# Kernel tuning notes

Hardware: AMD Instinct MI355X
Metric: run time of the kernel (lower is better)

The kernel has to match this reference:

```python
import jax, jax.numpy as jnp
import numpy as np

B, H, KVH, HD, S = 16, 32, 8, 128, 4096
D = H * HD  # 4096
Q = 1  # decode: one query token per batch element


def rotate_half(x):
    half = x.shape[-1] // 2
    return jnp.concatenate([-x[..., half:], x[..., :half]], axis=-1)


def setup_inputs() -> dict:
    key = jax.random.key(0)
    ks = jax.random.split(key, 8)
    hidden_states = jax.random.normal(ks[0], (B, Q, D), dtype=jnp.float32)
    current_steps = jax.random.randint(ks[1], (B,), 0, S - 1)
    # additive causal mask per batch: positions <= current_step visible
    pos = jnp.arange(S)[None, :]
    attention_mask = jnp.where(pos <= current_steps[:, None], 0.0, -1e9).astype(jnp.float32)[:, None, None, :]  # [B,1,1,S]
    # RoPE cos/sin at each batch element's current position
    inv_freq = 1.0 / (10000.0 ** (jnp.arange(0, HD, 2, dtype=jnp.float32) / HD))
    ang = current_steps[:, None].astype(jnp.float32) * inv_freq[None, :]  # [B, HD/2]
    ang = jnp.concatenate([ang, ang], axis=-1)  # [B, HD]
    cos = jnp.cos(ang)[:, None, None, :]  # [B,1,1,HD]
    sin = jnp.sin(ang)[:, None, None, :]
    past_key = jax.random.normal(ks[2], (B, KVH, S, HD), dtype=jnp.float32)
    past_value = jax.random.normal(ks[3], (B, KVH, S, HD), dtype=jnp.float32)
    sc = 1.0 / np.sqrt(D)
    Wq = jax.random.normal(ks[4], (D, H * HD), dtype=jnp.float32) * sc
    Wk = jax.random.normal(ks[5], (D, KVH * HD), dtype=jnp.float32) * sc
    Wv = jax.random.normal(ks[6], (D, KVH * HD), dtype=jnp.float32) * sc
    Wo = jax.random.normal(ks[7], (H * HD, D), dtype=jnp.float32) * sc
    return dict(hidden_states=hidden_states, attention_mask=attention_mask,
                current_steps=current_steps, cos=cos, sin=sin,
                past_key=past_key, past_value=past_value,
                Wq=Wq, Wk=Wk, Wv=Wv, Wo=Wo)


def reference(hidden_states, attention_mask, current_steps, cos, sin,
              past_key, past_value, Wq, Wk, Wv, Wo):
    b, q_len, d = hidden_states.shape
    # projections -> [B, heads, Q, HD]
    q = (hidden_states @ Wq).reshape(b, q_len, H, HD).transpose(0, 2, 1, 3)
    k = (hidden_states @ Wk).reshape(b, q_len, KVH, HD).transpose(0, 2, 1, 3)
    v = (hidden_states @ Wv).reshape(b, q_len, KVH, HD).transpose(0, 2, 1, 3)
    # RoPE
    q = q * cos + rotate_half(q) * sin
    k = k * cos + rotate_half(k) * sin
    # KV-cache scatter at current_step per batch (slice_scatter equivalent)
    def upd(cache_b, new_b, step):
        return jax.lax.dynamic_update_slice(cache_b, new_b, (0, step, 0))
    new_key = jax.vmap(upd)(past_key, k, current_steps)      # [B,KVH,S,HD]
    new_value = jax.vmap(upd)(past_value, v, current_steps)  # [B,KVH,S,HD]
    # GQA attention
    g = H // KVH
    qg = q.reshape(b, KVH, g, q_len, HD)
    scores = jnp.einsum('bkgqd,bksd->bkgqs', qg, new_key) / np.sqrt(HD)
    scores = scores + attention_mask[:, :, None, :, :]  # [B,1,1,Q,S] broadcast
    probs = jax.nn.softmax(scores, axis=-1)
    out = jnp.einsum('bkgqs,bksd->bkgqd', probs, new_value)
    out = out.reshape(b, H, q_len, HD).transpose(0, 2, 1, 3).reshape(b, q_len, H * HD)
    attn_out = out @ Wo
    return attn_out, new_key, new_value
```

## Files before the change

kernel.cpp:

```cpp
#include <hip/hip_runtime.h>

#define B 16
#define H 32
#define KVH 8
#define HD 128
#define S 4096
#define D 4096
#define NQKV 6144
#define PSPLIT 32
#define WSPLIT 32
#define NCH 16
#define CROWS (S / NCH)
#define SCALE 0.08838834764831845f

__global__ void k_proj(const float* __restrict__ hs, const float* __restrict__ Wq,
                       const float* __restrict__ Wk, const float* __restrict__ Wv,
                       float* __restrict__ part) {
  int n = blockIdx.x * 256 + threadIdx.x;
  int k0 = blockIdx.y * (D / PSPLIT);
  const float* w; int ldw, col;
  if (n < 4096)      { w = Wq; ldw = 4096; col = n; }
  else if (n < 5120) { w = Wk; ldw = 1024; col = n - 4096; }
  else               { w = Wv; ldw = 1024; col = n - 5120; }
  float acc[B];
#pragma unroll
  for (int b = 0; b < B; b++) acc[b] = 0.f;
  const float* wp = w + (size_t)k0 * ldw + col;
#pragma unroll 8
  for (int k = 0; k < D / PSPLIT; k++) {
    float wv = wp[(size_t)k * ldw];
#pragma unroll
    for (int b = 0; b < B; b++) acc[b] = fmaf(hs[b * D + k0 + k], wv, acc[b]);
  }
  float* p = part + (size_t)blockIdx.y * (B * NQKV);
#pragma unroll
  for (int b = 0; b < B; b++) p[(size_t)b * NQKV + n] = acc[b];
}

__global__ void k_reduce_rope(const float* __restrict__ part, const float* __restrict__ cosb,
                              const float* __restrict__ sinb, const int* __restrict__ steps,
                              float* __restrict__ qr, float* __restrict__ nkrow,
                              float* __restrict__ nvrow) {
  int i = blockIdx.x * 256 + threadIdx.x;
  int b = i / NQKV, n = i % NQKV;
  float v = 0.f;
#pragma unroll
  for (int c = 0; c < PSPLIT; c++) v += part[(size_t)c * B * NQKV + (size_t)b * NQKV + n];
  if (n < 5120) {
    int d = n & 127;
    int pn = (d < 64) ? n + 64 : n - 64;
    float pv = 0.f;
#pragma unroll
    for (int c = 0; c < PSPLIT; c++) pv += part[(size_t)c * B * NQKV + (size_t)b * NQKV + pn];
    float rot = (d < 64) ? -pv : pv;
    float r = v * cosb[b * HD + d] + rot * sinb[b * HD + d];
    if (n < 4096) qr[(size_t)b * D + n] = r;
    else          nkrow[(size_t)b * KVH * HD + (n - 4096)] = r;
  } else {
    nvrow[(size_t)b * KVH * HD + (n - 5120)] = v;
  }
}

__global__ void k_fusedK(const float* __restrict__ pastk, const float* __restrict__ nkrow,
                         const float* __restrict__ qr, const int* __restrict__ steps,
                         float* __restrict__ newk, float* __restrict__ scores) {
  int ch = blockIdx.x, kvh = blockIdx.y, b = blockIdx.z;
  int t = threadIdx.x;
  int ln = t & 15, rg = t >> 4;
  int s0 = ch * CROWS;
  int step = steps[b];
  int L = step + 1;
  int h0 = kvh * 4;
  const float4* qbase = (const float4*)(qr + ((size_t)b * H + h0) * HD);
  float4 q0[4], q1[4];
#pragma unroll
  for (int h = 0; h < 4; h++) {
    q0[h] = qbase[h * 32 + ln];
    q1[h] = qbase[h * 32 + ln + 16];
  }
  const float4* subp = (const float4*)(nkrow + (size_t)(b * KVH + kvh) * HD);
  float4 sub0 = subp[ln], sub1 = subp[ln + 16];
  const float4* src = (const float4*)(pastk + ((size_t)(b * KVH + kvh) * S + s0) * HD);
  float4*       dst = (float4*)(newk + ((size_t)(b * KVH + kvh) * S + s0) * HD);
  float* srow = scores + (size_t)(b * H + h0) * S + s0;
#pragma unroll 4
  for (int it = 0; it < CROWS / 16; ++it) {
    int row = it * 16 + rg;
    size_t o0 = (size_t)row * 32 + ln;
    float4 k0 = src[o0];
    float4 k1 = src[o0 + 16];
    if (s0 + row == step) { k0 = sub0; k1 = sub1; }
    dst[o0] = k0;
    dst[o0 + 16] = k1;
    if (s0 + row < L) {
      float a0, a1, a2, a3;
      a0 = fmaf(k0.x, q0[0].x, fmaf(k0.y, q0[0].y, fmaf(k0.z, q0[0].z, fmaf(k0.w, q0[0].w,
           fmaf(k1.x, q1[0].x, fmaf(k1.y, q1[0].y, fmaf(k1.z, q1[0].z, k1.w * q1[0].w)))))));
      a1 = fmaf(k0.x, q0[1].x, fmaf(k0.y, q0[1].y, fmaf(k0.z, q0[1].z, fmaf(k0.w, q0[1].w,
           fmaf(k1.x, q1[1].x, fmaf(k1.y, q1[1].y, fmaf(k1.z, q1[1].z, k1.w * q1[1].w)))))));
      a2 = fmaf(k0.x, q0[2].x, fmaf(k0.y, q0[2].y, fmaf(k0.z, q0[2].z, fmaf(k0.w, q0[2].w,
           fmaf(k1.x, q1[2].x, fmaf(k1.y, q1[2].y, fmaf(k1.z, q1[2].z, k1.w * q1[2].w)))))));
      a3 = fmaf(k0.x, q0[3].x, fmaf(k0.y, q0[3].y, fmaf(k0.z, q0[3].z, fmaf(k0.w, q0[3].w,
           fmaf(k1.x, q1[3].x, fmaf(k1.y, q1[3].y, fmaf(k1.z, q1[3].z, k1.w * q1[3].w)))))));
#pragma unroll
      for (int o = 1; o < 16; o <<= 1) {
        a0 += __shfl_xor(a0, o);
        a1 += __shfl_xor(a1, o);
        a2 += __shfl_xor(a2, o);
        a3 += __shfl_xor(a3, o);
      }
      if (ln < 4) {
        float my = (ln == 0) ? a0 : (ln == 1) ? a1 : (ln == 2) ? a2 : a3;
        srow[(size_t)ln * S + row] = my * SCALE;
      }
    }
  }
}

__global__ void k_smax(float* __restrict__ scores, const int* __restrict__ steps) {
  int bid = blockIdx.x;
  int b = bid >> 5, h = bid & 31;
  int t = threadIdx.x;
  __shared__ float red[4];
  int L = steps[b] + 1;
  float* srow = scores + (size_t)(b * H + h) * S;
  float lmax = -1e30f;
  for (int s = t; s < L; s += 256) lmax = fmaxf(lmax, srow[s]);
#pragma unroll
  for (int o = 32; o > 0; o >>= 1) lmax = fmaxf(lmax, __shfl_xor(lmax, o));
  if ((t & 63) == 0) red[t >> 6] = lmax;
  __syncthreads();
  float gm = fmaxf(fmaxf(red[0], red[1]), fmaxf(red[2], red[3]));
  float lsum = 0.f;
  for (int s = t; s < L; s += 256) {
    float p = __expf(srow[s] - gm);
    srow[s] = p;
    lsum += p;
  }
#pragma unroll
  for (int o = 32; o > 0; o >>= 1) lsum += __shfl_xor(lsum, o);
  __syncthreads();
  if ((t & 63) == 0) red[t >> 6] = lsum;
  __syncthreads();
  float inv = 1.f / (red[0] + red[1] + red[2] + red[3]);
  for (int s = t; s < L; s += 256) srow[s] *= inv;
}

__global__ void k_fusedV(const float* __restrict__ pastv, const float* __restrict__ nvrow,
                         const float* __restrict__ probs, const int* __restrict__ steps,
                         float* __restrict__ newv, float* __restrict__ part) {
  int ch = blockIdx.x, kvh = blockIdx.y, b = blockIdx.z;
  int t = threadIdx.x;
  int d4 = t & 31, rr = t >> 5;
  int s0 = ch * CROWS;
  int step = steps[b];
  int L = step + 1;
  int h0 = kvh * 4;
  float4 subv = ((const float4*)(nvrow + (size_t)(b * KVH + kvh) * HD))[d4];
  const float4* src = (const float4*)(pastv + ((size_t)(b * KVH + kvh) * S + s0) * HD);
  float4*       dst = (float4*)(newv + ((size_t)(b * KVH + kvh) * S + s0) * HD);
  const float* pb = probs + (size_t)(b * H + h0) * S + s0;
  float4 a0 = make_float4(0.f, 0.f, 0.f, 0.f), a1 = a0, a2 = a0, a3 = a0;
#pragma unroll 4
  for (int i = 0; i < CROWS / 8; ++i) {
    int r = i * 8 + rr;
    float4 v = src[r * 32 + d4];
    if (s0 + r == step) v = subv;
    dst[r * 32 + d4] = v;
    if (s0 + r < L) {
      float q0 = pb[r], q1 = pb[S + r], q2 = pb[2 * S + r], q3 = pb[3 * S + r];
      a0.x = fmaf(q0, v.x, a0.x); a0.y = fmaf(q0, v.y, a0.y);
      a0.z = fmaf(q0, v.z, a0.z); a0.w = fmaf(q0, v.w, a0.w);
      a1.x = fmaf(q1, v.x, a1.x); a1.y = fmaf(q1, v.y, a1.y);
      a1.z = fmaf(q1, v.z, a1.z); a1.w = fmaf(q1, v.w, a1.w);
      a2.x = fmaf(q2, v.x, a2.x); a2.y = fmaf(q2, v.y, a2.y);
      a2.z = fmaf(q2, v.z, a2.z); a2.w = fmaf(q2, v.w, a2.w);
      a3.x = fmaf(q3, v.x, a3.x); a3.y = fmaf(q3, v.y, a3.y);
      a3.z = fmaf(q3, v.z, a3.z); a3.w = fmaf(q3, v.w, a3.w);
    }
  }
  a0.x += __shfl_xor(a0.x, 32); a0.y += __shfl_xor(a0.y, 32);
  a0.z += __shfl_xor(a0.z, 32); a0.w += __shfl_xor(a0.w, 32);
  a1.x += __shfl_xor(a1.x, 32); a1.y += __shfl_xor(a1.y, 32);
  a1.z += __shfl_xor(a1.z, 32); a1.w += __shfl_xor(a1.w, 32);
  a2.x += __shfl_xor(a2.x, 32); a2.y += __shfl_xor(a2.y, 32);
  a2.z += __shfl_xor(a2.z, 32); a2.w += __shfl_xor(a2.w, 32);
  a3.x += __shfl_xor(a3.x, 32); a3.y += __shfl_xor(a3.y, 32);
  a3.z += __shfl_xor(a3.z, 32); a3.w += __shfl_xor(a3.w, 32);
  __shared__ float4 red[4][4][32];
  int w = t >> 6;
  if ((t & 32) == 0) {
    red[w][0][d4] = a0; red[w][1][d4] = a1; red[w][2][d4] = a2; red[w][3][d4] = a3;
  }
  __syncthreads();
  if (t < 128) {
    int hh = t >> 5, dd = t & 31;
    float4 x0 = red[0][hh][dd], x1 = red[1][hh][dd], x2 = red[2][hh][dd], x3 = red[3][hh][dd];
    float4 s;
    s.x = (x0.x + x1.x) + (x2.x + x3.x);
    s.y = (x0.y + x1.y) + (x2.y + x3.y);
    s.z = (x0.z + x1.z) + (x2.z + x3.z);
    s.w = (x0.w + x1.w) + (x2.w + x3.w);
    ((float4*)(part + (((size_t)ch * B + b) * KVH + kvh) * 512))[t] = s;
  }
}

__global__ void k_reduce_ctx(const float* __restrict__ part, float* __restrict__ ctx) {
  int i = blockIdx.x * 256 + threadIdx.x;
  int b = i >> 12, r = i & 4095, h = r >> 7, d = r & 127;
  int kvh = h >> 2, hl = h & 3;
  float s = 0.f;
#pragma unroll
  for (int c = 0; c < NCH; c++)
    s += part[(((size_t)c * B + b) * KVH + kvh) * 512 + hl * 128 + d];
  ctx[i] = s;
}

__global__ void k_wo(const float* __restrict__ ctx, const float* __restrict__ Wo,
                     float* __restrict__ part) {
  int n = blockIdx.x * 256 + threadIdx.x;
  int k0 = blockIdx.y * (D / WSPLIT);
  float acc[B];
#pragma unroll
  for (int b = 0; b < B; b++) acc[b] = 0.f;
  const float* wp = Wo + (size_t)k0 * D + n;
#pragma unroll 8
  for (int k = 0; k < D / WSPLIT; k++) {
    float wv = wp[(size_t)k * D];
#pragma unroll
    for (int b = 0; b < B; b++) acc[b] = fmaf(ctx[b * D + k0 + k], wv, acc[b]);
  }
  float* p = part + (size_t)blockIdx.y * (B * D);
#pragma unroll
  for (int b = 0; b < B; b++) p[(size_t)b * D + n] = acc[b];
}

__global__ void k_reduce_out(const float* __restrict__ part, float* __restrict__ out) {
  int i = blockIdx.x * 256 + threadIdx.x;
  float s = 0.f;
#pragma unroll
  for (int c = 0; c < WSPLIT; c++) s += part[(size_t)c * B * D + i];
  out[i] = s;
}

extern "C" void kernel_launch(void* const* d_in, const int* in_sizes, int n_in,
                              void* d_out, int out_size, void* d_ws, size_t ws_size,
                              hipStream_t stream) {
  const float* hs    = (const float*)d_in[0];
  const int*   steps = (const int*)d_in[2];
  const float* cosb  = (const float*)d_in[3];
  const float* sinb  = (const float*)d_in[4];
  const float* pk    = (const float*)d_in[5];
  const float* pvv   = (const float*)d_in[6];
  const float* Wq    = (const float*)d_in[7];
  const float* Wk    = (const float*)d_in[8];
  const float* Wv    = (const float*)d_in[9];
  const float* Wo    = (const float*)d_in[10];

  float* attn_out = (float*)d_out;
  float* newk = attn_out + (size_t)B * D;
  float* newv = newk + (size_t)B * KVH * S * HD;

  float* ws = (float*)d_ws;
  float* A        = ws;
  float* p_part   = A;
  float* p_scores = A;
  float* p_wopart = A;
  float* p_pvpart = A + 3145728;
  float* p_qr     = p_pvpart + 1048576;
  float* p_nkrow  = p_qr + (size_t)B * D;
  float* p_nvrow  = p_nkrow + (size_t)B * KVH * HD;
  float* p_ctx    = p_nvrow + (size_t)B * KVH * HD;

  hipLaunchKernelGGL(k_proj, dim3(NQKV / 256, PSPLIT), dim3(256), 0, stream,
                     hs, Wq, Wk, Wv, p_part);
  hipLaunchKernelGGL(k_reduce_rope, dim3(B * NQKV / 256), dim3(256), 0, stream,
                     p_part, cosb, sinb, steps, p_qr, p_nkrow, p_nvrow);
  hipLaunchKernelGGL(k_fusedK, dim3(NCH, KVH, B), dim3(256), 0, stream,
                     pk, p_nkrow, p_qr, steps, newk, p_scores);
  hipLaunchKernelGGL(k_smax, dim3(B * H), dim3(256), 0, stream,
                     p_scores, steps);
  hipLaunchKernelGGL(k_fusedV, dim3(NCH, KVH, B), dim3(256), 0, stream,
                     pvv, p_nvrow, p_scores, steps, newv, p_pvpart);
  hipLaunchKernelGGL(k_reduce_ctx, dim3(B * D / 256), dim3(256), 0, stream,
                     p_pvpart, p_ctx);
  hipLaunchKernelGGL(k_wo, dim3(D / 256, WSPLIT), dim3(256), 0, stream,
                     p_ctx, Wo, p_wopart);
  hipLaunchKernelGGL(k_reduce_out, dim3(B * D / 256), dim3(256), 0, stream,
                     p_wopart, attn_out);
}
```

Baseline: 343.4 us.

## Use nontemporal KV streaming and stage scores and probs through LDS

The K and V cache copy-and-attend kernels now read past KV and write new KV with nontemporal loads and stores, so the streaming traffic does less to pollute the caches. Scores are collected in a shared-memory tile and written out row-coalesced at the end of each chunk. Probabilities are preloaded into shared memory once per block instead of being fetched from global memory for every row. Per-row causal guards become wave-uniform per-iteration guards, which adds extra compute and some harmless garbage score writes past the valid length, plus extra barriers.

```diff
diff --git a/kernel.cpp b/kernel.cpp
--- a/kernel.cpp
+++ b/kernel.cpp
@@ -13,6 +13,17 @@
 #define CROWS (S / NCH)
 #define SCALE 0.08838834764831845f
 
+typedef float nfloat4 __attribute__((ext_vector_type(4)));
+
+__device__ __forceinline__ float4 ntload4(const float4* p) {
+  nfloat4 r = __builtin_nontemporal_load(reinterpret_cast<const nfloat4*>(p));
+  return *reinterpret_cast<float4*>(&r);
+}
+__device__ __forceinline__ void ntstore4(float4* p, float4 v) {
+  __builtin_nontemporal_store(*reinterpret_cast<nfloat4*>(&v),
+                              reinterpret_cast<nfloat4*>(p));
+}
+
 __global__ void k_proj(const float* __restrict__ hs, const float* __restrict__ Wq,
                        const float* __restrict__ Wk, const float* __restrict__ Wv,
                        float* __restrict__ part) {
@@ -67,6 +78,7 @@
   int ch = blockIdx.x, kvh = blockIdx.y, b = blockIdx.z;
   int t = threadIdx.x;
   int ln = t & 15, rg = t >> 4;
+  __shared__ float sbuf[CROWS][4];
   int s0 = ch * CROWS;
   int step = steps[b];
   int L = step + 1;
@@ -82,17 +94,16 @@
   float4 sub0 = subp[ln], sub1 = subp[ln + 16];
   const float4* src = (const float4*)(pastk + ((size_t)(b * KVH + kvh) * S + s0) * HD);
   float4*       dst = (float4*)(newk + ((size_t)(b * KVH + kvh) * S + s0) * HD);
-  float* srow = scores + (size_t)(b * H + h0) * S + s0;
 #pragma unroll 4
   for (int it = 0; it < CROWS / 16; ++it) {
     int row = it * 16 + rg;
     size_t o0 = (size_t)row * 32 + ln;
-    float4 k0 = src[o0];
-    float4 k1 = src[o0 + 16];
+    float4 k0 = ntload4(&src[o0]);
+    float4 k1 = ntload4(&src[o0 + 16]);
     if (s0 + row == step) { k0 = sub0; k1 = sub1; }
-    dst[o0] = k0;
-    dst[o0 + 16] = k1;
-    if (s0 + row < L) {
+    ntstore4(&dst[o0], k0);
+    ntstore4(&dst[o0 + 16], k1);
+    if (s0 + it * 16 < L) {
       float a0, a1, a2, a3;
       a0 = fmaf(k0.x, q0[0].x, fmaf(k0.y, q0[0].y, fmaf(k0.z, q0[0].z, fmaf(k0.w, q0[0].w,
            fmaf(k1.x, q1[0].x, fmaf(k1.y, q1[0].y, fmaf(k1.z, q1[0].z, k1.w * q1[0].w)))))));
@@ -111,9 +122,15 @@
       }
       if (ln < 4) {
         float my = (ln == 0) ? a0 : (ln == 1) ? a1 : (ln == 2) ? a2 : a3;
-        srow[(size_t)ln * S + row] = my * SCALE;
+        sbuf[row][ln] = my * SCALE;
       }
     }
+  }
+  if (s0 < L) {
+    __syncthreads();
+    float* srow = scores + (size_t)(b * H + h0) * S + s0;
+#pragma unroll
+    for (int j = 0; j < 4; ++j) srow[(size_t)j * S + t] = sbuf[t][j];
   }
 }
 
@@ -152,23 +169,31 @@
   int ch = blockIdx.x, kvh = blockIdx.y, b = blockIdx.z;
   int t = threadIdx.x;
   int d4 = t & 31, rr = t >> 5;
+  __shared__ float pbuf[CROWS][4];
   int s0 = ch * CROWS;
   int step = steps[b];
   int L = step + 1;
   int h0 = kvh * 4;
+  bool any = (s0 < L);
   float4 subv = ((const float4*)(nvrow + (size_t)(b * KVH + kvh) * HD))[d4];
   const float4* src = (const float4*)(pastv + ((size_t)(b * KVH + kvh) * S + s0) * HD);
   float4*       dst = (float4*)(newv + ((size_t)(b * KVH + kvh) * S + s0) * HD);
-  const float* pb = probs + (size_t)(b * H + h0) * S + s0;
+  if (any) {
+    const float* pb = probs + (size_t)(b * H + h0) * S + s0;
+#pragma unroll
+    for (int j = 0; j < 4; ++j)
+      pbuf[t][j] = (s0 + t < L) ? pb[(size_t)j * S + t] : 0.f;
+    __syncthreads();
+  }
   float4 a0 = make_float4(0.f, 0.f, 0.f, 0.f), a1 = a0, a2 = a0, a3 = a0;
 #pragma unroll 4
   for (int i = 0; i < CROWS / 8; ++i) {
     int r = i * 8 + rr;
-    float4 v = src[r * 32 + d4];
+    float4 v = ntload4(&src[r * 32 + d4]);
     if (s0 + r == step) v = subv;
-    dst[r * 32 + d4] = v;
-    if (s0 + r < L) {
-      float q0 = pb[r], q1 = pb[S + r], q2 = pb[2 * S + r], q3 = pb[3 * S + r];
+    ntstore4(&dst[r * 32 + d4], v);
+    if (any && i * 8 < L - s0) {
+      float q0 = pbuf[r][0], q1 = pbuf[r][1], q2 = pbuf[r][2], q3 = pbuf[r][3];
       a0.x = fmaf(q0, v.x, a0.x); a0.y = fmaf(q0, v.y, a0.y);
       a0.z = fmaf(q0, v.z, a0.z); a0.w = fmaf(q0, v.w, a0.w);
       a1.x = fmaf(q1, v.x, a1.x); a1.y = fmaf(q1, v.y, a1.y);
@@ -189,6 +214,7 @@
   a3.z += __shfl_xor(a3.z, 32); a3.w += __shfl_xor(a3.w, 32);
   __shared__ float4 red[4][4][32];
   int w = t >> 6;
+  __syncthreads();
   if ((t & 32) == 0) {
     red[w][0][d4] = a0; red[w][1][d4] = a1; red[w][2][d4] = a2; red[w][3][d4] = a3;
   }
```

Result: faster. 316.9 us (-7.7%).
